# Kernel optimization log

Hardware: AMD Instinct MI355X
Metric: run time of the kernel (lower is better)

Reference implementation:

```python
import jax, jax.numpy as jnp
import numpy as np

IN, ENC, H = 60, 32, 64  # input feat, encoder out, LSTM hidden per direction


def _lstm_scan(x_tbf, W_ih, W_hh, b):
    """x_tbf: [T,B,ENC]. Returns final (h, c), each [B,H]. PyTorch gate order i,f,g,o."""
    B = x_tbf.shape[1]
    h0 = jnp.zeros((B, H), x_tbf.dtype)
    c0 = jnp.zeros((B, H), x_tbf.dtype)

    def step(carry, x_t):
        h, c = carry
        gates = x_t @ W_ih.T + h @ W_hh.T + b  # [B, 4H]
        i, f, g, o = jnp.split(gates, 4, axis=-1)
        c = jax.nn.sigmoid(f) * c + jax.nn.sigmoid(i) * jnp.tanh(g)
        h = jax.nn.sigmoid(o) * jnp.tanh(c)
        return (h, c), None

    (h_fin, c_fin), _ = jax.lax.scan(step, (h0, c0), x_tbf)
    return h_fin, c_fin


def setup_inputs() -> dict:
    key = jax.random.key(0)
    ks = jax.random.split(key, 10)
    B, T = 256, 4096
    s_enc = 1.0 / np.sqrt(IN)
    s_lstm = 1.0 / np.sqrt(H)
    s_fin = 1.0 / np.sqrt(2 * H)
    return {
        "c": jax.random.normal(ks[0], (B, T, IN), jnp.float32),
        "W_enc": jax.random.uniform(ks[1], (ENC, IN), jnp.float32, -s_enc, s_enc),
        "b_enc": jax.random.uniform(ks[2], (ENC,), jnp.float32, -s_enc, s_enc),
        "W_ih_f": jax.random.uniform(ks[3], (4 * H, ENC), jnp.float32, -s_lstm, s_lstm),
        "W_hh_f": jax.random.uniform(ks[4], (4 * H, H), jnp.float32, -s_lstm, s_lstm),
        "b_f": jax.random.uniform(ks[5], (4 * H,), jnp.float32, -s_lstm, s_lstm),
        "W_ih_b": jax.random.uniform(ks[6], (4 * H, ENC), jnp.float32, -s_lstm, s_lstm),
        "W_hh_b": jax.random.uniform(ks[7], (4 * H, H), jnp.float32, -s_lstm, s_lstm),
        "b_b": jax.random.uniform(ks[8], (4 * H,), jnp.float32, -s_lstm, s_lstm),
        "W_fin": jax.random.uniform(ks[9], (3, 2 * H), jnp.float32, -s_fin, s_fin),
        "b_fin": jnp.zeros((3,), jnp.float32),
    }


def reference(c, W_enc, b_enc, W_ih_f, W_hh_f, b_f, W_ih_b, W_hh_b, b_b, W_fin, b_fin):
    # SequenceWise linear encoder: [B,T,60] -> [B,T,32]
    x = c @ W_enc.T + b_enc
    x_tbf = jnp.transpose(x, (1, 0, 2))  # [T,B,ENC]
    # Bidirectional LSTM; original code unpacks (h_n, c_n) as (c, h),
    # so it feeds the final CELL states into final_fc — reproduce that.
    _, c_fwd = _lstm_scan(x_tbf, W_ih_f, W_hh_f, b_f)
    _, c_bwd = _lstm_scan(x_tbf[::-1], W_ih_b, W_hh_b, b_b)
    hidden = jnp.concatenate([c_fwd, c_bwd], axis=1)  # [B, 2H]
    return hidden @ W_fin.T + b_fin  # [B, 3]
```

## Files before the change

kernel.cpp:

```cpp
#include <hip/hip_runtime.h>
#include <hip/hip_bf16.h>

#define T_LEN 4096

typedef __attribute__((ext_vector_type(8))) short bfrag8;
typedef __attribute__((ext_vector_type(4))) float f32x4;

__device__ __forceinline__ void wg_barrier() {
  asm volatile("s_waitcnt lgkmcnt(0)\ns_barrier" ::: "memory");
}

__device__ __forceinline__ float fact(float x, float S, float A, float B) {
  float e = __builtin_amdgcn_exp2f(S * x);
  return A + B * __builtin_amdgcn_rcpf(1.0f + e);
}
__device__ __forceinline__ float ftanh(float x) {
  float e = __builtin_amdgcn_exp2f(2.8853900817779268f * x);
  return 1.0f - 2.0f * __builtin_amdgcn_rcpf(1.0f + e);
}
template <int SEL>
__device__ __forceinline__ float qb(float v) {
  union { float f; int i; } u;
  u.f = v;
  u.i = __builtin_amdgcn_mov_dpp(u.i, SEL * 0x55, 0xF, 0xF, true);
  return u.f;
}

__global__ void prep_enc(const float* __restrict__ W_enc,
                         __hip_bfloat16* __restrict__ Wencb) {
  int u = threadIdx.x;
  if (u < 32) {
    for (int k = 0; k < 64; ++k)
      Wencb[u * 64 + k] = __float2bfloat16(k < 60 ? W_enc[u * 60 + k] : 0.0f);
  }
}

__global__ __launch_bounds__(256) void encoder(const float* __restrict__ c,
                                               const __hip_bfloat16* __restrict__ Wencb,
                                               __hip_bfloat16* __restrict__ x) {
  const int lane = threadIdx.x & 63, wave = threadIdx.x >> 6;
  const int q = lane >> 4, l15 = lane & 15;
  const size_t r0 = ((size_t)blockIdx.x * 4 + wave) * 16;

  bfrag8 bf00 = *(const bfrag8*)(Wencb + (0 * 16 + l15) * 64 + 0 * 32 + q * 8);
  bfrag8 bf01 = *(const bfrag8*)(Wencb + (0 * 16 + l15) * 64 + 1 * 32 + q * 8);
  bfrag8 bf10 = *(const bfrag8*)(Wencb + (1 * 16 + l15) * 64 + 0 * 32 + q * 8);
  bfrag8 bf11 = *(const bfrag8*)(Wencb + (1 * 16 + l15) * 64 + 1 * 32 + q * 8);

  const float* cr = c + (r0 + l15) * 60;
  float4 a0 = *(const float4*)(cr + q * 8);
  float4 a1 = *(const float4*)(cr + q * 8 + 4);
  float4 a2 = *(const float4*)(cr + 32 + q * 8);
  float4 a3 = (q == 3) ? float4{0.f, 0.f, 0.f, 0.f}
                       : *(const float4*)(cr + 36 + q * 8);
  union { bfrag8 v; __hip_bfloat16 h[8]; } A0, A1;
  A0.h[0] = __float2bfloat16(a0.x); A0.h[1] = __float2bfloat16(a0.y);
  A0.h[2] = __float2bfloat16(a0.z); A0.h[3] = __float2bfloat16(a0.w);
  A0.h[4] = __float2bfloat16(a1.x); A0.h[5] = __float2bfloat16(a1.y);
  A0.h[6] = __float2bfloat16(a1.z); A0.h[7] = __float2bfloat16(a1.w);
  A1.h[0] = __float2bfloat16(a2.x); A1.h[1] = __float2bfloat16(a2.y);
  A1.h[2] = __float2bfloat16(a2.z); A1.h[3] = __float2bfloat16(a2.w);
  A1.h[4] = __float2bfloat16(a3.x); A1.h[5] = __float2bfloat16(a3.y);
  A1.h[6] = __float2bfloat16(a3.z); A1.h[7] = __float2bfloat16(a3.w);

  f32x4 acc0 = {0.f, 0.f, 0.f, 0.f}, acc1 = {0.f, 0.f, 0.f, 0.f};
  acc0 = __builtin_amdgcn_mfma_f32_16x16x32_bf16(A0.v, bf00, acc0, 0, 0, 0);
  acc1 = __builtin_amdgcn_mfma_f32_16x16x32_bf16(A0.v, bf10, acc1, 0, 0, 0);
  acc0 = __builtin_amdgcn_mfma_f32_16x16x32_bf16(A1.v, bf01, acc0, 0, 0, 0);
  acc1 = __builtin_amdgcn_mfma_f32_16x16x32_bf16(A1.v, bf11, acc1, 0, 0, 0);

#pragma unroll
  for (int r = 0; r < 4; ++r) {
    size_t row = r0 + q * 4 + r;
    x[row * 32 + l15]      = __float2bfloat16(acc0[r]);
    x[row * 32 + 16 + l15] = __float2bfloat16(acc1[r]);
  }
}

__global__ void prep_weights(const float* __restrict__ b_enc,
                             const float* __restrict__ W_ih_f,
                             const float* __restrict__ W_hh_f,
                             const float* __restrict__ b_f,
                             const float* __restrict__ W_ih_b,
                             const float* __restrict__ W_hh_b,
                             const float* __restrict__ b_b,
                             __hip_bfloat16* __restrict__ Wc,
                             float* __restrict__ biasc) {
  const int dir = blockIdx.x;
  const int np = threadIdx.x;
  const int w = np >> 6, tile = (np >> 4) & 3, cc = np & 15;
  const int unit = w * 16 + tile * 4 + (cc >> 2);
  const int gate = cc & 3;
  const int no = gate * 64 + unit;
  const float* W_ih = dir ? W_ih_b : W_ih_f;
  const float* W_hh = dir ? W_hh_b : W_hh_f;
  const float* bv = dir ? b_b : b_f;
  __hip_bfloat16* row = Wc + (size_t)(dir * 256 + np) * 96;
#pragma unroll
  for (int k = 0; k < 32; ++k) row[k] = __float2bfloat16(W_ih[no * 32 + k]);
#pragma unroll
  for (int j = 0; j < 64; ++j) row[32 + j] = __float2bfloat16(W_hh[no * 64 + j]);
  float bb = bv[no];
#pragma unroll
  for (int e = 0; e < 32; ++e) bb += W_ih[no * 32 + e] * b_enc[e];
  biasc[dir * 256 + np] = bb;
}

__global__ __launch_bounds__(256, 2) void lstm_main(
    const __hip_bfloat16* __restrict__ x, const __hip_bfloat16* __restrict__ Wc,
    const float* __restrict__ biasc, float* __restrict__ cfin) {
  __shared__ short Hbuf[2][64];

  const int tid = threadIdx.x, lane = tid & 63, wave = tid >> 6;
  const int quad = lane >> 4, l15 = lane & 15;
  const int g = lane & 3;
  const int unit = wave * 16 + quad * 4 + (l15 >> 2);
  const int dir = (int)blockIdx.x & 1;
  const int b = (int)blockIdx.x >> 1;

  bfrag8 wf[4][3];
  float bias[4];
#pragma unroll
  for (int tl = 0; tl < 4; ++tl) {
    const int np = wave * 64 + tl * 16 + l15;
    const __hip_bfloat16* wr = Wc + (size_t)(dir * 256 + np) * 96 + quad * 8;
#pragma unroll
    for (int kt = 0; kt < 3; ++kt) wf[tl][kt] = *(const bfrag8*)(wr + kt * 32);
    bias[tl] = biasc[dir * 256 + np];
  }

  const bool isg = (g == 2);
  const float S = isg ? 2.8853900817779268f : -1.4426950408889634f;
  const float Aa = isg ? 1.0f : 0.0f;
  const float Bb = isg ? -2.0f : 1.0f;

  const __hip_bfloat16* xr = x + (size_t)b * T_LEN * 32 + quad * 8;

  if (tid < 128) ((short*)Hbuf)[tid] = 0;

  bfrag8 xb[4];
#pragma unroll
  for (int qq = 0; qq < 4; ++qq) {
    int tp = dir ? (T_LEN - 1 - qq) : qq;
    xb[qq] = *(const bfrag8*)(xr + (size_t)tp * 32);
  }

  float cst = 0.f;
  wg_barrier();

#pragma unroll 4
  for (int t = 0; t < T_LEN; ++t) {
    const int cur = t & 1;
    bfrag8 ahA = *(const bfrag8*)&Hbuf[cur][quad * 8];
    bfrag8 ahB = *(const bfrag8*)&Hbuf[cur][32 + quad * 8];
    f32x4 ax0 = {bias[0], bias[0], bias[0], bias[0]};
    f32x4 ax1 = {bias[1], bias[1], bias[1], bias[1]};
    f32x4 ax2 = {bias[2], bias[2], bias[2], bias[2]};
    f32x4 ax3 = {bias[3], bias[3], bias[3], bias[3]};
    ax0 = __builtin_amdgcn_mfma_f32_16x16x32_bf16(xb[t & 3], wf[0][0], ax0, 0, 0, 0);
    ax1 = __builtin_amdgcn_mfma_f32_16x16x32_bf16(xb[t & 3], wf[1][0], ax1, 0, 0, 0);
    ax2 = __builtin_amdgcn_mfma_f32_16x16x32_bf16(xb[t & 3], wf[2][0], ax2, 0, 0, 0);
    ax3 = __builtin_amdgcn_mfma_f32_16x16x32_bf16(xb[t & 3], wf[3][0], ax3, 0, 0, 0);
    f32x4 ah0 = {0.f, 0.f, 0.f, 0.f}, ah1 = {0.f, 0.f, 0.f, 0.f};
    f32x4 ah2 = {0.f, 0.f, 0.f, 0.f}, ah3 = {0.f, 0.f, 0.f, 0.f};
    ah0 = __builtin_amdgcn_mfma_f32_16x16x32_bf16(ahA, wf[0][1], ah0, 0, 0, 0);
    ah1 = __builtin_amdgcn_mfma_f32_16x16x32_bf16(ahA, wf[1][1], ah1, 0, 0, 0);
    ah2 = __builtin_amdgcn_mfma_f32_16x16x32_bf16(ahA, wf[2][1], ah2, 0, 0, 0);
    ah3 = __builtin_amdgcn_mfma_f32_16x16x32_bf16(ahA, wf[3][1], ah3, 0, 0, 0);
    ah0 = __builtin_amdgcn_mfma_f32_16x16x32_bf16(ahB, wf[0][2], ah0, 0, 0, 0);
    ah1 = __builtin_amdgcn_mfma_f32_16x16x32_bf16(ahB, wf[1][2], ah1, 0, 0, 0);
    ah2 = __builtin_amdgcn_mfma_f32_16x16x32_bf16(ahB, wf[2][2], ah2, 0, 0, 0);
    ah3 = __builtin_amdgcn_mfma_f32_16x16x32_bf16(ahB, wf[3][2], ah3, 0, 0, 0);
    {
      int tn = t + 4; if (tn > T_LEN - 1) tn = T_LEN - 1;
      int tp = dir ? (T_LEN - 1 - tn) : tn;
      xb[t & 3] = *(const bfrag8*)(xr + (size_t)tp * 32);
    }
    float vx01 = (quad & 1) ? ax1[0] : ax0[0];
    float vx23 = (quad & 1) ? ax3[0] : ax2[0];
    float vx = (quad & 2) ? vx23 : vx01;
    float vh01 = (quad & 1) ? ah1[0] : ah0[0];
    float vh23 = (quad & 1) ? ah3[0] : ah2[0];
    float vh = (quad & 2) ? vh23 : vh01;
    float a = fact(vx + vh, S, Aa, Bb);
    float gi = qb<0>(a), gf = qb<1>(a), gg = qb<2>(a), go = qb<3>(a);
    cst = gf * cst + gi * gg;
    float h = go * ftanh(cst);
    if (g == 0) *(__hip_bfloat16*)&Hbuf[cur ^ 1][unit] = __float2bfloat16(h);
    wg_barrier();
  }

  if (g == 0) {
    cfin[(size_t)(dir * 256 + b) * 64 + unit] = cst;
  }
}

__global__ void final_fc(const float* __restrict__ cfin,
                         const float* __restrict__ W_fin,
                         const float* __restrict__ b_fin,
                         float* __restrict__ out) {
  int b = threadIdx.x;
  const float* cf = cfin + (size_t)b * 64;
  const float* cb = cfin + (size_t)(256 + b) * 64;
  float a0 = b_fin[0], a1 = b_fin[1], a2 = b_fin[2];
  for (int u = 0; u < 64; ++u) {
    float vf = cf[u], vb = cb[u];
    a0 += W_fin[0 * 128 + u] * vf + W_fin[0 * 128 + 64 + u] * vb;
    a1 += W_fin[1 * 128 + u] * vf + W_fin[1 * 128 + 64 + u] * vb;
    a2 += W_fin[2 * 128 + u] * vf + W_fin[2 * 128 + 64 + u] * vb;
  }
  out[b * 3 + 0] = a0;
  out[b * 3 + 1] = a1;
  out[b * 3 + 2] = a2;
}

extern "C" void kernel_launch(void* const* d_in, const int* in_sizes, int n_in,
                              void* d_out, int out_size, void* d_ws, size_t ws_size,
                              hipStream_t stream) {
  (void)in_sizes; (void)n_in; (void)out_size; (void)ws_size;
  const float* c      = (const float*)d_in[0];
  const float* W_enc  = (const float*)d_in[1];
  const float* b_enc  = (const float*)d_in[2];
  const float* W_ih_f = (const float*)d_in[3];
  const float* W_hh_f = (const float*)d_in[4];
  const float* b_f    = (const float*)d_in[5];
  const float* W_ih_b = (const float*)d_in[6];
  const float* W_hh_b = (const float*)d_in[7];
  const float* b_b    = (const float*)d_in[8];
  const float* W_fin  = (const float*)d_in[9];
  const float* b_fin  = (const float*)d_in[10];
  float* out = (float*)d_out;

  char* ws = (char*)d_ws;
  __hip_bfloat16* x     = (__hip_bfloat16*)ws;
  __hip_bfloat16* Wc    = (__hip_bfloat16*)(ws + 67108864);
  float* biasc          = (float*)(ws + 67108864 + 98304);
  __hip_bfloat16* Wencb = (__hip_bfloat16*)(ws + 67108864 + 100352);
  float* cfin           = (float*)(ws + 67108864 + 104448);

  prep_enc<<<1, 32, 0, stream>>>(W_enc, Wencb);
  prep_weights<<<2, 256, 0, stream>>>(b_enc, W_ih_f, W_hh_f, b_f,
                                      W_ih_b, W_hh_b, b_b, Wc, biasc);
  encoder<<<16384, 256, 0, stream>>>(c, Wencb, x);
  lstm_main<<<512, 256, 0, stream>>>(x, Wc, biasc, cfin);
  final_fc<<<1, 256, 0, stream>>>(cfin, W_fin, b_fin, out);
}
```

Measured before the change: 1.574 ms.

## Process two batch sequences per LSTM block using spare MFMA rows

Each block now runs the recurrence for two batch elements at once. It uses two rows of the 16-row MFMA tile for two sequences, keeps two cell states per lane and widens the shared hidden buffer to hold both hidden vectors. This halves the grid to 256 blocks and removes the 2-blocks-per-CU launch bound, so each CU runs one block instead of two interleaved recurrences. The x and h MFMA products are also accumulated into a single chain instead of separate accumulators. The aim is to amortize the per-step MFMA, barrier and activation work across two sequences, at the cost of a slightly longer dependent MFMA chain per step.

```diff
diff --git a/kernel.cpp b/kernel.cpp
--- a/kernel.cpp
+++ b/kernel.cpp
@@ -106,17 +106,17 @@
   biasc[dir * 256 + np] = bb;
 }
 
-__global__ __launch_bounds__(256, 2) void lstm_main(
+__global__ __launch_bounds__(256) void lstm_main(
     const __hip_bfloat16* __restrict__ x, const __hip_bfloat16* __restrict__ Wc,
     const float* __restrict__ biasc, float* __restrict__ cfin) {
-  __shared__ short Hbuf[2][64];
+  __shared__ short Hbuf[2][144];
 
   const int tid = threadIdx.x, lane = tid & 63, wave = tid >> 6;
   const int quad = lane >> 4, l15 = lane & 15;
   const int g = lane & 3;
   const int unit = wave * 16 + quad * 4 + (l15 >> 2);
   const int dir = (int)blockIdx.x & 1;
-  const int b = (int)blockIdx.x >> 1;
+  const int b0 = ((int)blockIdx.x >> 1) << 1;
 
   bfrag8 wf[4][3];
   float bias[4];
@@ -134,9 +134,10 @@
   const float Aa = isg ? 1.0f : 0.0f;
   const float Bb = isg ? -2.0f : 1.0f;
 
-  const __hip_bfloat16* xr = x + (size_t)b * T_LEN * 32 + quad * 8;
-
-  if (tid < 128) ((short*)Hbuf)[tid] = 0;
+  const __hip_bfloat16* xr = x + (size_t)(b0 + (l15 & 1)) * T_LEN * 32 + quad * 8;
+  const int hrd = (l15 & 1) * 72 + quad * 8;
+
+  if (tid < 288) ((short*)Hbuf)[tid] = 0;
 
   bfrag8 xb[4];
 #pragma unroll
@@ -145,53 +146,53 @@
     xb[qq] = *(const bfrag8*)(xr + (size_t)tp * 32);
   }
 
-  float cst = 0.f;
+  float cst0 = 0.f, cst1 = 0.f;
   wg_barrier();
 
 #pragma unroll 4
   for (int t = 0; t < T_LEN; ++t) {
     const int cur = t & 1;
-    bfrag8 ahA = *(const bfrag8*)&Hbuf[cur][quad * 8];
-    bfrag8 ahB = *(const bfrag8*)&Hbuf[cur][32 + quad * 8];
-    f32x4 ax0 = {bias[0], bias[0], bias[0], bias[0]};
-    f32x4 ax1 = {bias[1], bias[1], bias[1], bias[1]};
-    f32x4 ax2 = {bias[2], bias[2], bias[2], bias[2]};
-    f32x4 ax3 = {bias[3], bias[3], bias[3], bias[3]};
-    ax0 = __builtin_amdgcn_mfma_f32_16x16x32_bf16(xb[t & 3], wf[0][0], ax0, 0, 0, 0);
-    ax1 = __builtin_amdgcn_mfma_f32_16x16x32_bf16(xb[t & 3], wf[1][0], ax1, 0, 0, 0);
-    ax2 = __builtin_amdgcn_mfma_f32_16x16x32_bf16(xb[t & 3], wf[2][0], ax2, 0, 0, 0);
-    ax3 = __builtin_amdgcn_mfma_f32_16x16x32_bf16(xb[t & 3], wf[3][0], ax3, 0, 0, 0);
-    f32x4 ah0 = {0.f, 0.f, 0.f, 0.f}, ah1 = {0.f, 0.f, 0.f, 0.f};
-    f32x4 ah2 = {0.f, 0.f, 0.f, 0.f}, ah3 = {0.f, 0.f, 0.f, 0.f};
-    ah0 = __builtin_amdgcn_mfma_f32_16x16x32_bf16(ahA, wf[0][1], ah0, 0, 0, 0);
-    ah1 = __builtin_amdgcn_mfma_f32_16x16x32_bf16(ahA, wf[1][1], ah1, 0, 0, 0);
-    ah2 = __builtin_amdgcn_mfma_f32_16x16x32_bf16(ahA, wf[2][1], ah2, 0, 0, 0);
-    ah3 = __builtin_amdgcn_mfma_f32_16x16x32_bf16(ahA, wf[3][1], ah3, 0, 0, 0);
-    ah0 = __builtin_amdgcn_mfma_f32_16x16x32_bf16(ahB, wf[0][2], ah0, 0, 0, 0);
-    ah1 = __builtin_amdgcn_mfma_f32_16x16x32_bf16(ahB, wf[1][2], ah1, 0, 0, 0);
-    ah2 = __builtin_amdgcn_mfma_f32_16x16x32_bf16(ahB, wf[2][2], ah2, 0, 0, 0);
-    ah3 = __builtin_amdgcn_mfma_f32_16x16x32_bf16(ahB, wf[3][2], ah3, 0, 0, 0);
+    bfrag8 ahA = *(const bfrag8*)&Hbuf[cur][hrd];
+    bfrag8 ahB = *(const bfrag8*)&Hbuf[cur][hrd + 32];
+    f32x4 a0 = {bias[0], bias[0], bias[0], bias[0]};
+    f32x4 a1 = {bias[1], bias[1], bias[1], bias[1]};
+    f32x4 a2 = {bias[2], bias[2], bias[2], bias[2]};
+    f32x4 a3 = {bias[3], bias[3], bias[3], bias[3]};
+    a0 = __builtin_amdgcn_mfma_f32_16x16x32_bf16(xb[t & 3], wf[0][0], a0, 0, 0, 0);
+    a1 = __builtin_amdgcn_mfma_f32_16x16x32_bf16(xb[t & 3], wf[1][0], a1, 0, 0, 0);
+    a2 = __builtin_amdgcn_mfma_f32_16x16x32_bf16(xb[t & 3], wf[2][0], a2, 0, 0, 0);
+    a3 = __builtin_amdgcn_mfma_f32_16x16x32_bf16(xb[t & 3], wf[3][0], a3, 0, 0, 0);
+    a0 = __builtin_amdgcn_mfma_f32_16x16x32_bf16(ahA, wf[0][1], a0, 0, 0, 0);
+    a1 = __builtin_amdgcn_mfma_f32_16x16x32_bf16(ahA, wf[1][1], a1, 0, 0, 0);
+    a2 = __builtin_amdgcn_mfma_f32_16x16x32_bf16(ahA, wf[2][1], a2, 0, 0, 0);
+    a3 = __builtin_amdgcn_mfma_f32_16x16x32_bf16(ahA, wf[3][1], a3, 0, 0, 0);
+    a0 = __builtin_amdgcn_mfma_f32_16x16x32_bf16(ahB, wf[0][2], a0, 0, 0, 0);
+    a1 = __builtin_amdgcn_mfma_f32_16x16x32_bf16(ahB, wf[1][2], a1, 0, 0, 0);
+    a2 = __builtin_amdgcn_mfma_f32_16x16x32_bf16(ahB, wf[2][2], a2, 0, 0, 0);
+    a3 = __builtin_amdgcn_mfma_f32_16x16x32_bf16(ahB, wf[3][2], a3, 0, 0, 0);
     {
       int tn = t + 4; if (tn > T_LEN - 1) tn = T_LEN - 1;
       int tp = dir ? (T_LEN - 1 - tn) : tn;
       xb[t & 3] = *(const bfrag8*)(xr + (size_t)tp * 32);
     }
-    float vx01 = (quad & 1) ? ax1[0] : ax0[0];
-    float vx23 = (quad & 1) ? ax3[0] : ax2[0];
-    float vx = (quad & 2) ? vx23 : vx01;
-    float vh01 = (quad & 1) ? ah1[0] : ah0[0];
-    float vh23 = (quad & 1) ? ah3[0] : ah2[0];
-    float vh = (quad & 2) ? vh23 : vh01;
-    float a = fact(vx + vh, S, Aa, Bb);
-    float gi = qb<0>(a), gf = qb<1>(a), gg = qb<2>(a), go = qb<3>(a);
-    cst = gf * cst + gi * gg;
-    float h = go * ftanh(cst);
-    if (g == 0) *(__hip_bfloat16*)&Hbuf[cur ^ 1][unit] = __float2bfloat16(h);
+    float v0 = (quad & 2) ? ((quad & 1) ? a3[0] : a2[0]) : ((quad & 1) ? a1[0] : a0[0]);
+    float v1 = (quad & 2) ? ((quad & 1) ? a3[1] : a2[1]) : ((quad & 1) ? a1[1] : a0[1]);
+    float av0 = fact(v0, S, Aa, Bb);
+    float av1 = fact(v1, S, Aa, Bb);
+    float i0 = qb<0>(av0), f0 = qb<1>(av0), g0v = qb<2>(av0), o0 = qb<3>(av0);
+    float i1 = qb<0>(av1), f1 = qb<1>(av1), g1v = qb<2>(av1), o1 = qb<3>(av1);
+    cst0 = f0 * cst0 + i0 * g0v;
+    cst1 = f1 * cst1 + i1 * g1v;
+    float h0 = o0 * ftanh(cst0);
+    float h1 = o1 * ftanh(cst1);
+    short* hb = Hbuf[cur ^ 1];
+    if (g == 0) *(__hip_bfloat16*)&hb[unit] = __float2bfloat16(h0);
+    if (g == 1) *(__hip_bfloat16*)&hb[72 + unit] = __float2bfloat16(h1);
     wg_barrier();
   }
 
-  if (g == 0) {
-    cfin[(size_t)(dir * 256 + b) * 64 + unit] = cst;
+  if (g < 2) {
+    cfin[(size_t)(dir * 256 + b0 + g) * 64 + unit] = g ? cst1 : cst0;
   }
 }
 
@@ -242,6 +243,6 @@
   prep_weights<<<2, 256, 0, stream>>>(b_enc, W_ih_f, W_hh_f, b_f,
                                       W_ih_b, W_hh_b, b_b, Wc, biasc);
   encoder<<<16384, 256, 0, stream>>>(c, Wencb, x);
-  lstm_main<<<512, 256, 0, stream>>>(x, Wc, biasc, cfin);
+  lstm_main<<<256, 256, 0, stream>>>(x, Wc, biasc, cfin);
   final_fc<<<1, 256, 0, stream>>>(cfin, W_fin, b_fin, out);
 }
```

New measurement: 1.700 ms. +8.0%, slower.
